# Kernel optimization log

Hardware: AMD Instinct MI355X
Metric: run time of the kernel (lower is better)

The kernel has to match this reference:

```python
import jax, jax.numpy as jnp
import numpy as np

B, N, C, H, D, M = 8, 4096, 512, 8, 64, 16
TOPK = 3
TAU = 0.1
DIV_REG = 0.01


def setup_inputs() -> dict:
    key = jax.random.key(0)
    ks = jax.random.split(key, 12)
    w = lambda i, shape: 0.02 * jax.random.normal(ks[i], shape, dtype=jnp.float32)
    return {
        "x": jax.random.normal(ks[0], (B, N, C), dtype=jnp.float32),
        "W_qkv": w(1, (C, 3 * C)),                    # qkv_bias=False
        "W_proj": w(2, (C, C)), "b_proj": jnp.zeros((C,), jnp.float32),
        "W_rspec": w(3, (C, H * M)), "b_rspec": jnp.zeros((H * M,), jnp.float32),
        "W_rspat": w(4, (C, H * M)), "b_rspat": jnp.zeros((H * M,), jnp.float32),
        "K_spec": w(5, (H, M, D)),                    # prototype banks (EMA buffers)
        "K_spat": w(6, (H, M, D)),
        "W_tok": w(7, (D, D)), "b_tok": jnp.zeros((D,), jnp.float32),
        "W_prot": w(8, (D, D)), "b_prot": jnp.zeros((D,), jnp.float32),
    }


def topk_mask_from_logits(logits, k):
    # keep top-k of softmax probs along last axis, renormalize
    vals = jax.lax.top_k(logits, k)[0]
    thresh = vals[..., -1:]
    mask = (logits >= thresh).astype(logits.dtype)
    probs = jax.nn.softmax(logits, axis=-1) * mask
    denom = jnp.maximum(jnp.sum(probs, axis=-1, keepdims=True), 1e-6)
    return probs / denom


def _l2norm(a, eps):
    return a / jnp.maximum(jnp.linalg.norm(a, axis=-1, keepdims=True), eps)


def reference(x, W_qkv, W_proj, b_proj, W_rspec, b_rspec, W_rspat, b_rspat,
              K_spec, K_spat, W_tok, b_tok, W_prot, b_prot):
    # qkv: [B,N,3C] -> q,k,v each [B,H,N,D]
    qkv = (x @ W_qkv).reshape(B, N, 3, H, D).transpose(2, 0, 3, 1, 4)
    q, _k, v = qkv[0], qkv[1], qkv[2]

    # routing logits [B,H,N,M] -> top-k masked probs
    r_spec = topk_mask_from_logits(
        (x @ W_rspec + b_rspec).reshape(B, N, H, M).transpose(0, 2, 1, 3), TOPK)
    r_spat = topk_mask_from_logits(
        (x @ W_rspat + b_rspat).reshape(B, N, H, M).transpose(0, 2, 1, 3), TOPK)

    # effective keys from prototype banks: [B,H,N,D]
    K_eff = (jnp.einsum('bhnm,hmd->bhnd', r_spec, K_spec)
             + jnp.einsum('bhnm,hmd->bhnd', r_spat, K_spat))
    K_norm = jax.nn.softmax(K_eff, axis=-2)          # softmax over tokens N

    # linear attention reorder: context [B,H,D,D], then Q @ context
    context = jnp.einsum('bhnd,bhne->bhde', K_norm, v)
    out = jnp.einsum('bhnd,bhde->bhne', q, context)  # note: scale unused in source
    out = out.transpose(0, 2, 1, 3).reshape(B, N, C) @ W_proj + b_proj

    # ---- contrastive aux loss ----
    t_n = _l2norm(v @ W_tok + b_tok, 1e-12)          # [B,H,N,D]
    p_spec_n = _l2norm(K_spec @ W_prot + b_prot, 1e-12)
    p_spat_n = _l2norm(K_spat @ W_prot + b_prot, 1e-12)
    sim_spec = jnp.einsum('bhnd,hmd->bhnm', t_n, p_spec_n)
    sim_spat = jnp.einsum('bhnd,hmd->bhnm', t_n, p_spat_n)
    pos_spec = jnp.sum(sim_spec * r_spec, axis=-1)
    pos_spat = jnp.sum(sim_spat * r_spat, axis=-1)
    loss_spec = -jnp.mean(pos_spec / TAU - jax.nn.logsumexp(sim_spec / TAU, axis=-1))
    loss_spat = -jnp.mean(pos_spat / TAU - jax.nn.logsumexp(sim_spat / TAU, axis=-1))
    contrastive_loss = 0.5 * (loss_spec + loss_spat)

    def diversity_loss(P):
        h, m, _d = P.shape
        p = P / jnp.maximum(jnp.linalg.norm(P, axis=-1, keepdims=True), 1e-6)
        sim = jnp.einsum('hmd,hnd->hmn', p, p)
        mask = 1.0 - jnp.eye(m, dtype=P.dtype)[None]
        return jnp.sum(sim * mask) / (h * m * (m - 1) + 1e-6)

    diversity = DIV_REG * (diversity_loss(K_spec) + diversity_loss(K_spat))
    return out, contrastive_loss, diversity
```

## Files before the change

kernel.cpp:

```cpp
#include <hip/hip_runtime.h>
#include <math.h>

#define B_ 8
#define N_ 4096
#define C_ 512
#define H_ 8
#define D_ 64
#define M_ 16
#define BN_TOK (B_*N_)
#define TAU_ 0.1f

typedef short s8v __attribute__((ext_vector_type(8)));
typedef float f4v __attribute__((ext_vector_type(4)));
typedef unsigned short u16;

__device__ __forceinline__ float wave_reduce_sum(float v){
  #pragma unroll
  for (int o = 32; o > 0; o >>= 1) v += __shfl_xor(v, o);
  return v;
}

__device__ __forceinline__ unsigned short f2b(float f){
  unsigned int u = __float_as_uint(f);
  u += 0x7fffu + ((u >> 16) & 1u);
  return (unsigned short)(u >> 16);
}

__device__ __forceinline__ float b2f(u16 b){
  return __uint_as_float(((unsigned int)b) << 16);
}

__device__ __forceinline__ s8v pack8(const float* f){
  s8v r;
  #pragma unroll
  for (int e = 0; e < 8; ++e) r[e] = (short)f2b(f[e]);
  return r;
}

__device__ __forceinline__ void gload16(const u16* g, u16* l){
  __builtin_amdgcn_global_load_lds(
      (const __attribute__((address_space(1))) unsigned int*)g,
      (__attribute__((address_space(3))) unsigned int*)l, 16, 0, 0);
}

__global__ __launch_bounds__(256) void prep_all(const float* __restrict__ x, u16* __restrict__ xb,
                                                const float* __restrict__ W_qkv,
                                                const float* __restrict__ W_rspec,
                                                const float* __restrict__ W_rspat,
                                                const float* __restrict__ W_proj,
                                                u16* __restrict__ Wqk,
                                                u16* __restrict__ Wt_v,
                                                u16* __restrict__ Wt_r,
                                                u16* __restrict__ Wt_p){
  const int bid = blockIdx.x;
  const int t = threadIdx.x;
  if (bid < 1024) {
    const int n8 = (BN_TOK*C_)/8;
    for (int i = bid * 256 + t; i < n8; i += 1024*256) {
      const float4* p = (const float4*)(x + (size_t)i * 8);
      float4 a = p[0], b = p[1];
      float f[8] = {a.x,a.y,a.z,a.w,b.x,b.y,b.z,b.w};
      *(s8v*)(xb + (size_t)i * 8) = pack8(f);
    }
    return;
  }
  if (bid < 1536) {
    const int k = bid - 1024;
    Wqk[(size_t)k*512 + t]       = f2b(W_qkv[(size_t)k*1536 + t]);
    Wqk[(size_t)k*512 + t + 256] = f2b(W_qkv[(size_t)k*1536 + t + 256]);
    return;
  }
  const int r = bid - 1536;
  const float* src; int ld, coff, n; u16* dst;
  if (r < 512)       { src = W_qkv;   ld = 1536; coff = 1024; n = r;        dst = Wt_v; }
  else if (r < 640)  { src = W_rspec; ld = 128;  coff = 0;    n = r - 512;  dst = Wt_r; }
  else if (r < 768)  { src = W_rspat; ld = 128;  coff = 0;    n = r - 640;  dst = Wt_r + 128*512; }
  else               { src = W_proj;  ld = 512;  coff = 0;    n = r - 768;  dst = Wt_p; }
  dst[(size_t)n*512 + t]       = f2b(src[(size_t)t*ld + coff + n]);
  dst[(size_t)n*512 + t + 256] = f2b(src[(size_t)(t+256)*ld + coff + n]);
}

template<int MODE>
__global__ __launch_bounds__(256) void gemm_bt(const u16* __restrict__ A,
                                               const u16* __restrict__ Bt,
                                               const float* __restrict__ bias,
                                               void* __restrict__ C,
                                               u16* __restrict__ C2,
                                               int K, int lda, int ldc, int ldc2,
                                               int split, int bt_bstride) {
  __shared__ __align__(16) u16 Asm[2][2][128*32];
  __shared__ __align__(16) u16 Bsm[2][2][128*32];
  const int tid = threadIdx.x;
  const int lane = tid & 63, w = tid >> 6;
  const int bm = blockIdx.x * 128, bn = blockIdx.y * 128;

  const int lrow = lane >> 2;
  const int kch  = ((lane & 3) ^ ((lane >> 3) & 3)) << 3;

  const u16* Btb = Bt + (size_t)(bm >> 12) * bt_bstride;
  const u16* Ag0 = A   + (size_t)(bm + w*16 + lrow) * lda + kch;
  const u16* Ag1 = Ag0 + (size_t)64 * lda;
  const u16* Bg0 = Btb + (size_t)(bn + w*16 + lrow) * K + kch;
  const u16* Bg1 = Bg0 + (size_t)64 * K;
  const int l0 = (w*16)*32, l1 = (w*16+64)*32;

  const int lm = lane & 15, lg = lane >> 4;
  const int w0 = (w >> 1) * 64, c0 = (w & 1) * 64;
  const int xs = (lg ^ ((lm >> 1) & 3)) << 3;

  const int NSTEP = K >> 6;

  f4v acc[4][4];
  #pragma unroll
  for (int i = 0; i < 4; ++i)
    #pragma unroll
    for (int j = 0; j < 4; ++j) acc[i][j] = (f4v){0.f,0.f,0.f,0.f};

  #define STAGE(buf, tt)                                        \
    gload16(Ag0 + (tt)*64,      &Asm[buf][0][l0]);              \
    gload16(Ag1 + (tt)*64,      &Asm[buf][0][l1]);              \
    gload16(Ag0 + (tt)*64 + 32, &Asm[buf][1][l0]);              \
    gload16(Ag1 + (tt)*64 + 32, &Asm[buf][1][l1]);              \
    gload16(Bg0 + (tt)*64,      &Bsm[buf][0][l0]);              \
    gload16(Bg1 + (tt)*64,      &Bsm[buf][0][l1]);              \
    gload16(Bg0 + (tt)*64 + 32, &Bsm[buf][1][l0]);              \
    gload16(Bg1 + (tt)*64 + 32, &Bsm[buf][1][l1]);

  STAGE(0, 0)
  STAGE(1, 1)

  int cur = 0;
  for (int k = 0; k < NSTEP; ++k) {
    if (k < NSTEP - 1) asm volatile("s_waitcnt vmcnt(8)" ::: "memory");
    else               asm volatile("s_waitcnt vmcnt(0)" ::: "memory");
    __builtin_amdgcn_s_barrier();
    __builtin_amdgcn_sched_barrier(0);

    #pragma unroll
    for (int h = 0; h < 2; ++h) {
      s8v af[4], bf_[4];
      #pragma unroll
      for (int i = 0; i < 4; ++i) af[i]  = *(const s8v*)&Asm[cur][h][(w0 + 16*i + lm)*32 + xs];
      #pragma unroll
      for (int j = 0; j < 4; ++j) bf_[j] = *(const s8v*)&Bsm[cur][h][(c0 + 16*j + lm)*32 + xs];
      #pragma unroll
      for (int i = 0; i < 4; ++i)
        #pragma unroll
        for (int j = 0; j < 4; ++j)
          acc[i][j] = __builtin_amdgcn_mfma_f32_16x16x32_bf16(af[i], bf_[j], acc[i][j], 0, 0, 0);
    }

    __builtin_amdgcn_sched_barrier(0);
    __builtin_amdgcn_s_barrier();
    if (k + 2 < NSTEP) {
      STAGE(cur, k + 2)
    }
    __builtin_amdgcn_sched_barrier(0);
    cur ^= 1;
  }
  #undef STAGE

  #pragma unroll
  for (int j = 0; j < 4; ++j) {
    const int col = bn + c0 + 16*j + lm;
    const float bj = (MODE == 0 && bias) ? bias[col] : 0.f;
    #pragma unroll
    for (int i = 0; i < 4; ++i) {
      const int row = bm + w0 + 16*i + 4*lg;
      #pragma unroll
      for (int r = 0; r < 4; ++r) {
        if (MODE == 2 && bn >= split)
          C2[(size_t)(row + r) * ldc2 + (col - split)] = f2b(acc[i][j][r]);
        else if (MODE == 1 || MODE == 2)
          ((u16*)C)[(size_t)(row + r) * ldc + col] = f2b(acc[i][j][r]);
        else
          ((float*)C)[(size_t)(row + r) * ldc + col] = acc[i][j][r] + bj;
      }
    }
  }
}

__global__ __launch_bounds__(256) void router_topk(const u16* __restrict__ logits,
                            const float* __restrict__ b_rspec, const float* __restrict__ b_rspat,
                            u16* __restrict__ rb_spec, u16* __restrict__ rb_spat) {
  int t = blockIdx.x * blockDim.x + threadIdx.x;
  if (t >= BN_TOK * H_ * 2) return;
  int route = t & 1, h = (t >> 1) & 7, bn = t >> 4;
  int b = bn >> 12, n = bn & 4095;
  const u16* lg = logits + (size_t)bn*256 + route*128 + h*16;
  const float* bias = (route ? b_rspat : b_rspec) + h*16;
  float v[16];
  #pragma unroll
  for (int m=0;m<16;++m) v[m] = b2f(lg[m]) + bias[m];
  float m1=-1e30f, m2=-1e30f, m3=-1e30f;
  #pragma unroll
  for (int m=0;m<16;++m){
    float x=v[m];
    if (x>m1){m3=m2;m2=m1;m1=x;}
    else if (x>m2){m3=m2;m2=x;}
    else if (x>m3){m3=x;}
  }
  float S=0.f, Sm=0.f, e[16];
  #pragma unroll
  for (int m=0;m<16;++m){ e[m]=expf(v[m]-m1); S+=e[m]; if (v[m]>=m3) Sm+=e[m]; }
  float denom = fmaxf(Sm/S, 1e-6f);
  float inv = 1.f/(S*denom);
  size_t idx = (((size_t)b*H_ + h)*N_ + n)*16;
  u16* rb  = (route ? rb_spat : rb_spec) + idx;
  #pragma unroll
  for (int m=0;m<16;++m) {
    float val = (v[m] >= m3) ? e[m]*inv : 0.f;
    rb[m] = f2b(val);
  }
}

__global__ __launch_bounds__(256) void context_mfma(const u16* __restrict__ rb_spec, const u16* __restrict__ rb_spat,
                               const float* __restrict__ K_spec, const float* __restrict__ K_spat,
                               const u16* __restrict__ vb, u16* __restrict__ pctx, float* __restrict__ pZ) {
  const int chunk = blockIdx.x & 15, bh = blockIdx.x >> 4;
  const int b = bh >> 3, h = bh & 7;
  const int tid = threadIdx.x;
  const int lane = tid & 63, w = tid >> 6;
  const int lm = lane & 15, lg = lane >> 4;

  __shared__ __align__(16) unsigned short Kc[64*32];
  __shared__ __align__(16) unsigned short Rs[64*32];
  __shared__ __align__(16) unsigned short Vt[64*64];
  __shared__ __align__(16) unsigned short Ps[64*64];
  __shared__ float Zs[256];

  {
    int d = tid & 63, c = tid >> 6;
    float f[8];
    #pragma unroll
    for (int u = 0; u < 8; ++u) {
      int k = c*8 + u;
      f[u] = (k < 16) ? K_spec[h*1024 + k*64 + d] : K_spat[h*1024 + (k-16)*64 + d];
    }
    *(s8v*)&Kc[d*32 + ((c ^ (d&3)) << 3)] = pack8(f);
  }

  const u16* rsg = rb_spec + ((size_t)bh*N_ + chunk*256)*16;
  const u16* rtg = rb_spat + ((size_t)bh*N_ + chunk*256)*16;
  const u16* vbase = vb + h*64;
  const size_t tokbase = (size_t)b*N_ + chunk*256;

  f4v acc2[4];
  #pragma unroll
  for (int j = 0; j < 4; ++j) acc2[j] = (f4v){0.f,0.f,0.f,0.f};
  float zreg[4] = {0.f,0.f,0.f,0.f};

  for (int t0 = 0; t0 < 4; ++t0) {
    __syncthreads();
    {
      int n = tid & 63, c = tid >> 6;
      const u16* src = (c < 2 ? rsg : rtg) + ((size_t)(t0*64 + n))*16 + (c&1)*8;
      *(s8v*)&Rs[n*32 + ((c ^ (n&3)) << 3)] = *(const s8v*)src;
    }
    {
      int n = tid & 63, eq = tid >> 6;
      const u16* src = vbase + (tokbase + t0*64 + n)*512 + eq*16;
      u16 f[16];
      *(s8v*)&f[0] = ((const s8v*)src)[0];
      *(s8v*)&f[8] = ((const s8v*)src)[1];
      #pragma unroll
      for (int u = 0; u < 16; ++u) {
        int e = eq*16 + u;
        Vt[e*64 + ((((n>>3) ^ (e&7)) << 3) | (n&7))] = f[u];
      }
    }
    __syncthreads();
    {
      s8v a1 = *(const s8v*)&Rs[(16*w + lm)*32 + ((lg ^ (lm&3)) << 3)];
      #pragma unroll
      for (int j = 0; j < 4; ++j) {
        s8v b1 = *(const s8v*)&Kc[(16*j + lm)*32 + ((lg ^ (lm&3)) << 3)];
        f4v c1 = (f4v){0.f,0.f,0.f,0.f};
        c1 = __builtin_amdgcn_mfma_f32_16x16x32_bf16(a1, b1, c1, 0, 0, 0);
        float p0 = expf(c1[0]), p1 = expf(c1[1]), p2 = expf(c1[2]), p3 = expf(c1[3]);
        float zz = p0 + p1 + p2 + p3;
        zz += __shfl_xor(zz, 16); zz += __shfl_xor(zz, 32);
        zreg[j] += zz;
        int d = 16*j + lm;
        int n0w = 16*w + 4*lg;
        Ps[d*64 + (((((n0w  )>>3) ^ (d&7)) << 3) | ((n0w  )&7))] = f2b(p0);
        Ps[d*64 + (((((n0w+1)>>3) ^ (d&7)) << 3) | ((n0w+1)&7))] = f2b(p1);
        Ps[d*64 + (((((n0w+2)>>3) ^ (d&7)) << 3) | ((n0w+2)&7))] = f2b(p2);
        Ps[d*64 + (((((n0w+3)>>3) ^ (d&7)) << 3) | ((n0w+3)&7))] = f2b(p3);
      }
    }
    __syncthreads();
    #pragma unroll
    for (int kb = 0; kb < 2; ++kb) {
      s8v a2 = *(const s8v*)&Vt[(16*w + lm)*64 + (((kb*4 + lg) ^ (lm&7)) << 3)];
      #pragma unroll
      for (int j = 0; j < 4; ++j) {
        s8v b2 = *(const s8v*)&Ps[(16*j + lm)*64 + (((kb*4 + lg) ^ (lm&7)) << 3)];
        acc2[j] = __builtin_amdgcn_mfma_f32_16x16x32_bf16(a2, b2, acc2[j], 0, 0, 0);
      }
    }
  }
  u16* pc = pctx + (size_t)(bh*16 + chunk)*4096;
  #pragma unroll
  for (int j = 0; j < 4; ++j) {
    #pragma unroll
    for (int r = 0; r < 4; ++r)
      pc[(16*w + 4*lg + r)*64 + 16*j + lm] = f2b(acc2[j][r]);
    if (lg == 0) Zs[w*64 + 16*j + lm] = zreg[j];
  }
  __syncthreads();
  if (tid < 64)
    pZ[(size_t)(bh*16 + chunk)*64 + tid] = Zs[tid] + Zs[64+tid] + Zs[128+tid] + Zs[192+tid];
}

__global__ __launch_bounds__(256) void context_reduce(const u16* __restrict__ pctx, const float* __restrict__ pZ,
                              float* __restrict__ ctx) {
  const int gid = blockIdx.x * 256 + threadIdx.x;
  const int bh = gid >> 12, e = (gid >> 6) & 63, d = gid & 63;
  float z = 0.f, s = 0.f;
  for (int c = 0; c < 16; ++c) {
    z += pZ[(size_t)(bh*16 + c)*64 + d];
    s += b2f(pctx[(size_t)(bh*16 + c)*4096 + e*64 + d]);
  }
  ctx[(size_t)bh*4096 + e*64 + d] = s / z;
}

__global__ __launch_bounds__(256) void cwt_kernel(const float* __restrict__ ctx, const u16* __restrict__ Wt_p,
                                                  u16* __restrict__ CWt) {
  const int bh = blockIdx.x >> 3, oct = blockIdx.x & 7;
  const int b = bh >> 3, h = bh & 7;
  const int tid = threadIdx.x;
  __shared__ float ctxS[64*64];
  __shared__ u16 WsL[64*64];
  {
    int e = tid >> 2, dq = tid & 3;
    const float4* src = (const float4*)(ctx + (size_t)bh*4096 + e*64 + dq*16);
    float4* dst = (float4*)(ctxS + e*64 + dq*16);
    dst[0] = src[0]; dst[1] = src[1]; dst[2] = src[2]; dst[3] = src[3];
  }
  const int c0 = oct * 64;
  {
    int cl = tid >> 2, eq = tid & 3;
    const s8v* src = (const s8v*)(Wt_p + (size_t)(c0 + cl)*512 + h*64 + eq*16);
    *(s8v*)&WsL[cl*64 + eq*16]     = src[0];
    *(s8v*)&WsL[cl*64 + eq*16 + 8] = src[1];
  }
  __syncthreads();
  const int d = tid & 63, cq = tid >> 6;
  for (int ci = 0; ci < 16; ++ci) {
    int cl = cq*16 + ci;
    float acc = 0.f;
    #pragma unroll
    for (int e = 0; e < 64; ++e)
      acc = fmaf(ctxS[e*64 + d], b2f(WsL[cl*64 + e]), acc);
    CWt[((size_t)b*512 + (c0 + cl))*512 + h*64 + d] = f2b(acc);
  }
}

__global__ __launch_bounds__(64) void protnorm_div(const float* __restrict__ K_spec, const float* __restrict__ K_spat,
                               const float* __restrict__ W_prot, const float* __restrict__ b_prot,
                               float* __restrict__ pnorm, float* __restrict__ pdiv) {
  const int bid = blockIdx.x;
  const int e = threadIdx.x;
  if (bid < 256) {
    int route = bid >> 7, hm = bid & 127;
    const float* Km = (route ? K_spat : K_spec) + hm*64;
    __shared__ float kv[64];
    kv[e] = Km[e];
    __syncthreads();
    float acc = b_prot[e];
    for (int dcol = 0; dcol < 64; ++dcol) acc = fmaf(kv[dcol], W_prot[dcol*64 + e], acc);
    float n2 = wave_reduce_sum(acc*acc);
    pnorm[(size_t)bid*64 + e] = acc / fmaxf(sqrtf(n2), 1e-12f);
    return;
  }
  const int db = bid - 256;
  int route = db >> 3, h = db & 7;
  const float* Km = (route ? K_spat : K_spec) + h*16*64;
  float s = 0.f, selfsum = 0.f;
  for (int m = 0; m < 16; ++m) {
    float x = Km[m*64 + e];
    float n2 = wave_reduce_sum(x*x);
    float p = x / fmaxf(sqrtf(n2), 1e-6f);
    s += p; selfsum += p*p;
  }
  float off = wave_reduce_sum(s*s - selfsum);
  if (e == 0) pdiv[db] = off;
}

__global__ __launch_bounds__(256) void contrastive_mfma(const u16* __restrict__ vb,
                                   const u16* __restrict__ rb_spec, const u16* __restrict__ rb_spat,
                                   const float* __restrict__ W_tok, const float* __restrict__ b_tok,
                                   const float* __restrict__ pnorm, float* __restrict__ pcontr) {
  const int tile = blockIdx.x & 255;
  const int h = blockIdx.x >> 8;
  const int t0 = tile * 128;
  const int b = t0 >> 12;
  const int n0 = t0 & 4095;
  const int tid = threadIdx.x;
  const int lane = tid & 63, w = tid >> 6;
  const int lm = lane & 15, lg = lane >> 4;

  __shared__ __align__(16) unsigned short Usm[128*72];
  __shared__ __align__(16) unsigned short Wsm[64*72];
  __shared__ __align__(16) unsigned short Psm[32*72];
  __shared__ float nrmS[128];
  __shared__ float btkS[64];
  __shared__ float bred[2][4];
  float* Uf = (float*)Usm;

  {
    const int vr = tid >> 1, vh = tid & 1;
    const u16* vg = vb + (size_t)(b*N_ + n0 + vr)*512 + h*64 + vh*32;
    #pragma unroll
    for (int c = 0; c < 4; ++c) *(s8v*)&Usm[vr*72 + vh*32 + c*8] = ((const s8v*)vg)[c];
  }
  {
    const int e = tid & 63, kh = tid >> 6;
    float f[16];
    #pragma unroll
    for (int rr = 0; rr < 16; ++rr) f[rr] = W_tok[(size_t)(kh*16+rr)*64 + e];
    *(s8v*)&Wsm[e*72 + kh*16]     = pack8(&f[0]);
    *(s8v*)&Wsm[e*72 + kh*16 + 8] = pack8(&f[8]);
  }
  if (tid < 128) {
    const int proto = tid >> 2, q4 = tid & 3;
    const int src = (proto < 16) ? (h*16 + proto) : (128 + h*16 + (proto-16));
    const float* pg = pnorm + (size_t)src*64 + q4*16;
    float f[16];
    #pragma unroll
    for (int i = 0; i < 4; ++i) {
      float4 v4 = ((const float4*)pg)[i];
      f[4*i]=v4.x; f[4*i+1]=v4.y; f[4*i+2]=v4.z; f[4*i+3]=v4.w;
    }
    *(s8v*)&Psm[proto*72 + q4*16]     = pack8(&f[0]);
    *(s8v*)&Psm[proto*72 + q4*16 + 8] = pack8(&f[8]);
  }
  if (tid < 64) btkS[tid] = b_tok[tid];
  __syncthreads();

  f4v acc[2][4];
  #pragma unroll
  for (int i=0;i<2;++i)
    #pragma unroll
    for (int j=0;j<4;++j) acc[i][j] = (f4v){0.f,0.f,0.f,0.f};
  {
    s8v bf0[4], bf1[4];
    #pragma unroll
    for (int j=0;j<4;++j) {
      bf0[j] = *(const s8v*)&Wsm[(j*16+lm)*72 + lg*8];
      bf1[j] = *(const s8v*)&Wsm[(j*16+lm)*72 + 32 + lg*8];
    }
    #pragma unroll
    for (int i=0;i<2;++i) {
      s8v af0 = *(const s8v*)&Usm[(w*32+16*i+lm)*72 + lg*8];
      s8v af1 = *(const s8v*)&Usm[(w*32+16*i+lm)*72 + 32 + lg*8];
      #pragma unroll
      for (int j=0;j<4;++j) {
        acc[i][j] = __builtin_amdgcn_mfma_f32_16x16x32_bf16(af0, bf0[j], acc[i][j], 0, 0, 0);
        acc[i][j] = __builtin_amdgcn_mfma_f32_16x16x32_bf16(af1, bf1[j], acc[i][j], 0, 0, 0);
      }
    }
  }
  #pragma unroll
  for (int i=0;i<2;++i) {
    #pragma unroll
    for (int r=0;r<4;++r) {
      float s = 0.f;
      #pragma unroll
      for (int j=0;j<4;++j) {
        float val = acc[i][j][r] + btkS[j*16+lm];
        acc[i][j][r] = val;
        s += val*val;
      }
      s += __shfl_xor(s,1); s += __shfl_xor(s,2); s += __shfl_xor(s,4); s += __shfl_xor(s,8);
      if (lm == 0) nrmS[w*32 + 16*i + lg*4 + r] = s;
    }
  }
  #pragma unroll
  for (int i=0;i<2;++i)
    #pragma unroll
    for (int j=0;j<4;++j)
      #pragma unroll
      for (int r=0;r<4;++r)
        Usm[(w*32+16*i+lg*4+r)*72 + j*16+lm] = f2b(acc[i][j][r]);
  __syncthreads();

  f4v acc2[2][2];
  #pragma unroll
  for (int i=0;i<2;++i)
    #pragma unroll
    for (int j=0;j<2;++j) acc2[i][j] = (f4v){0.f,0.f,0.f,0.f};
  {
    s8v bf0[2], bf1[2];
    #pragma unroll
    for (int j=0;j<2;++j) {
      bf0[j] = *(const s8v*)&Psm[(j*16+lm)*72 + lg*8];
      bf1[j] = *(const s8v*)&Psm[(j*16+lm)*72 + 32 + lg*8];
    }
    #pragma unroll
    for (int i=0;i<2;++i) {
      s8v af0 = *(const s8v*)&Usm[(w*32+16*i+lm)*72 + lg*8];
      s8v af1 = *(const s8v*)&Usm[(w*32+16*i+lm)*72 + 32 + lg*8];
      #pragma unroll
      for (int j=0;j<2;++j) {
        acc2[i][j] = __builtin_amdgcn_mfma_f32_16x16x32_bf16(af0, bf0[j], acc2[i][j], 0, 0, 0);
        acc2[i][j] = __builtin_amdgcn_mfma_f32_16x16x32_bf16(af1, bf1[j], acc2[i][j], 0, 0, 0);
      }
    }
  }
  #pragma unroll
  for (int i=0;i<2;++i)
    #pragma unroll
    for (int j=0;j<2;++j)
      #pragma unroll
      for (int r=0;r<4;++r)
        Uf[(w*32+16*i+lg*4+r)*36 + j*16+lm] = acc2[i][j][r];
  __syncthreads();

  float l = 0.f;
  {
    const int tt = tid >> 1, route = tid & 1;
    float inv = 1.f / fmaxf(sqrtf(nrmS[tt]), 1e-12f);
    const u16* rg = (route ? rb_spat : rb_spec) + (((size_t)b*H_ + h)*N_ + n0 + tt)*16;
    float s0[16];
    #pragma unroll
    for (int m=0;m<16;++m) s0[m] = Uf[tt*36 + route*16 + m]*inv;
    float pos = 0.f, mx = -1e30f;
    #pragma unroll
    for (int m=0;m<16;++m) {
      pos += s0[m]*b2f(rg[m]);
      mx = fmaxf(mx, s0[m]);
    }
    float z = 0.f;
    #pragma unroll
    for (int m=0;m<16;++m) z += expf((s0[m]-mx)/TAU_);
    l = pos/TAU_ - (mx/TAU_ + logf(z));
  }
  float lspec = (tid & 1) ? 0.f : l;
  float lspat = (tid & 1) ? l : 0.f;
  lspec = wave_reduce_sum(lspec);
  lspat = wave_reduce_sum(lspat);
  if (lane == 0) { bred[0][w]=lspec; bred[1][w]=lspat; }
  __syncthreads();
  if (tid == 0) {
    pcontr[2*blockIdx.x]     = bred[0][0]+bred[0][1]+bred[0][2]+bred[0][3];
    pcontr[2*blockIdx.x + 1] = bred[1][0]+bred[1][1]+bred[1][2]+bred[1][3];
  }
}

__global__ __launch_bounds__(256) void finalize_kernel(const float* __restrict__ pcontr,
                                                       const float* __restrict__ pdiv,
                                                       float* __restrict__ tail) {
  __shared__ float red[2][4];
  const int tid = threadIdx.x, lane = tid & 63, w = tid >> 6;
  float ls = 0.f, lt = 0.f;
  for (int k = tid; k < 2048; k += 256) { ls += pcontr[2*k]; lt += pcontr[2*k + 1]; }
  ls = wave_reduce_sum(ls);
  lt = wave_reduce_sum(lt);
  if (lane == 0) { red[0][w] = ls; red[1][w] = lt; }
  __syncthreads();
  if (tid == 0) {
    float sspec = red[0][0]+red[0][1]+red[0][2]+red[0][3];
    float sspat = red[1][0]+red[1][1]+red[1][2]+red[1][3];
    float dspec = 0.f, dspat = 0.f;
    for (int k = 0; k < 8; ++k) { dspec += pdiv[k]; dspat += pdiv[8+k]; }
    float loss_spec = -(sspec / (float)(B_*H_*N_));
    float loss_spat = -(sspat / (float)(B_*H_*N_));
    float denom = (float)(H_*M_*(M_-1)) + 1e-6f;
    tail[0] = 0.5f*(loss_spec + loss_spat);
    tail[1] = 0.01f * (dspec/denom + dspat/denom);
  }
}

extern "C" void kernel_launch(void* const* d_in, const int* in_sizes, int n_in,
                              void* d_out, int out_size, void* d_ws, size_t ws_size,
                              hipStream_t stream) {
  const float* x       = (const float*)d_in[0];
  const float* W_qkv   = (const float*)d_in[1];
  const float* W_proj  = (const float*)d_in[2];
  const float* b_proj  = (const float*)d_in[3];
  const float* W_rspec = (const float*)d_in[4];
  const float* b_rspec = (const float*)d_in[5];
  const float* W_rspat = (const float*)d_in[6];
  const float* b_rspat = (const float*)d_in[7];
  const float* K_spec  = (const float*)d_in[8];
  const float* K_spat  = (const float*)d_in[9];
  const float* W_tok   = (const float*)d_in[10];
  const float* b_tok   = (const float*)d_in[11];
  const float* W_prot  = (const float*)d_in[12];
  const float* b_prot  = (const float*)d_in[13];
  float* out = (float*)d_out;

  float* ws = (float*)d_ws;
  u16*   vb      = (u16*)ws;
  u16*   logits  = (u16*)(ws + 8388608);
  u16*   pctx    = (u16*)(ws + 8388608);
  float* pZ      = ws + 8388608 + 4194304;
  u16*   rb_spec = (u16*)(ws + 12648448);
  u16*   rb_spat = (u16*)(ws + 14745600);
  u16*   xb      = (u16*)(ws + 16842752);
  u16*   Wqk     = (u16*)(ws + 25231360);
  u16*   Wt_v    = (u16*)(ws + 25362432);
  u16*   Wt_r    = (u16*)(ws + 25493504);
  u16*   Wt_p    = (u16*)(ws + 25559040);
  float* ctxb    = ws + 25690112;
  float* pnorm   = ws + 25952256;
  float* pcontr  = ws + 25968640;
  float* pdiv    = ws + 25972736;
  u16*   CWt     = (u16*)(ws + 25972752);
  u16*   W2t     = (u16*)(ws + 27021328);

  dim3 blk256(256);

  prep_all<<<2816, blk256, 0, stream>>>(x, xb, W_qkv, W_rspec, W_rspat, W_proj, Wqk, Wt_v, Wt_r, Wt_p);

  gemm_bt<2><<<dim3(256,6), blk256, 0, stream>>>(xb, Wt_v, nullptr, vb, logits,
                                                 512, 512, 512, 256, 512, 0);
  router_topk<<<2048, blk256, 0, stream>>>(logits, b_rspec, b_rspat, rb_spec, rb_spat);
  context_mfma<<<1024, blk256, 0, stream>>>(rb_spec, rb_spat, K_spec, K_spat, vb, pctx, pZ);
  context_reduce<<<1024, blk256, 0, stream>>>(pctx, pZ, ctxb);
  cwt_kernel<<<512, blk256, 0, stream>>>(ctxb, Wt_p, CWt);
  gemm_bt<1><<<dim3(32,4), blk256, 0, stream>>>(CWt, Wqk, nullptr, W2t, nullptr,
                                                512, 512, 512, 0, 1 << 30, 0);
  protnorm_div<<<272, dim3(64), 0, stream>>>(K_spec, K_spat, W_prot, b_prot, pnorm, pdiv);
  contrastive_mfma<<<2048, blk256, 0, stream>>>(vb, rb_spec, rb_spat, W_tok, b_tok, pnorm, pcontr);
  gemm_bt<0><<<dim3(256,4), blk256, 0, stream>>>(xb, W2t, b_proj, out, nullptr,
                                                 512, 512, 512, 0, 1 << 30, 512*512);
  finalize_kernel<<<1, blk256, 0, stream>>>(pcontr, pdiv, out + 16777216);
}
```

Before: 306.0 us.

## Fuse router top-k into consumers and fold context reduction into cwt kernel

Removes the standalone router_topk kernel. The top-k softmax routing weights are now recomputed from the bf16 logits inside both context_mfma and contrastive_mfma. The context_reduce kernel is also dropped: cwt_kernel sums the 16 partial contexts and normalizers itself and applies 1/Z at the output. This cuts two launches and the round trip of the routing and context buffers through global memory, at the cost of computing top-k twice and doing a strided gather of the partials in cwt_kernel. The workspace is re-laid out so pctx no longer aliases logits, which are now still read later.

Result: slower. 314.7 us (+2.9%).

```diff
diff --git a/kernel.cpp b/kernel.cpp
--- a/kernel.cpp
+++ b/kernel.cpp
@@ -35,6 +35,24 @@
   #pragma unroll
   for (int e = 0; e < 8; ++e) r[e] = (short)f2b(f[e]);
   return r;
+}
+
+__device__ __forceinline__ void topk16(const float* v, float* out){
+  float m1=-1e30f, m2=-1e30f, m3=-1e30f;
+  #pragma unroll
+  for (int m=0;m<16;++m){
+    float x=v[m];
+    if (x>m1){m3=m2;m2=m1;m1=x;}
+    else if (x>m2){m3=m2;m2=x;}
+    else if (x>m3){m3=x;}
+  }
+  float S=0.f, Sm=0.f, e[16];
+  #pragma unroll
+  for (int m=0;m<16;++m){ e[m]=expf(v[m]-m1); S+=e[m]; if (v[m]>=m3) Sm+=e[m]; }
+  float denom = fmaxf(Sm/S, 1e-6f);
+  float inv = 1.f/(S*denom);
+  #pragma unroll
+  for (int m=0;m<16;++m) out[m] = (v[m] >= m3) ? e[m]*inv : 0.f;
 }
 
 __device__ __forceinline__ void gload16(const u16* g, u16* l){
@@ -180,41 +198,8 @@
   }
 }
 
-__global__ __launch_bounds__(256) void router_topk(const u16* __restrict__ logits,
-                            const float* __restrict__ b_rspec, const float* __restrict__ b_rspat,
-                            u16* __restrict__ rb_spec, u16* __restrict__ rb_spat) {
-  int t = blockIdx.x * blockDim.x + threadIdx.x;
-  if (t >= BN_TOK * H_ * 2) return;
-  int route = t & 1, h = (t >> 1) & 7, bn = t >> 4;
-  int b = bn >> 12, n = bn & 4095;
-  const u16* lg = logits + (size_t)bn*256 + route*128 + h*16;
-  const float* bias = (route ? b_rspat : b_rspec) + h*16;
-  float v[16];
-  #pragma unroll
-  for (int m=0;m<16;++m) v[m] = b2f(lg[m]) + bias[m];
-  float m1=-1e30f, m2=-1e30f, m3=-1e30f;
-  #pragma unroll
-  for (int m=0;m<16;++m){
-    float x=v[m];
-    if (x>m1){m3=m2;m2=m1;m1=x;}
-    else if (x>m2){m3=m2;m2=x;}
-    else if (x>m3){m3=x;}
-  }
-  float S=0.f, Sm=0.f, e[16];
-  #pragma unroll
-  for (int m=0;m<16;++m){ e[m]=expf(v[m]-m1); S+=e[m]; if (v[m]>=m3) Sm+=e[m]; }
-  float denom = fmaxf(Sm/S, 1e-6f);
-  float inv = 1.f/(S*denom);
-  size_t idx = (((size_t)b*H_ + h)*N_ + n)*16;
-  u16* rb  = (route ? rb_spat : rb_spec) + idx;
-  #pragma unroll
-  for (int m=0;m<16;++m) {
-    float val = (v[m] >= m3) ? e[m]*inv : 0.f;
-    rb[m] = f2b(val);
-  }
-}
-
-__global__ __launch_bounds__(256) void context_mfma(const u16* __restrict__ rb_spec, const u16* __restrict__ rb_spat,
+__global__ __launch_bounds__(256) void context_mfma(const u16* __restrict__ logits,
+                               const float* __restrict__ b_rspec, const float* __restrict__ b_rspat,
                                const float* __restrict__ K_spec, const float* __restrict__ K_spat,
                                const u16* __restrict__ vb, u16* __restrict__ pctx, float* __restrict__ pZ) {
   const int chunk = blockIdx.x & 15, bh = blockIdx.x >> 4;
@@ -224,7 +209,7 @@
   const int lm = lane & 15, lg = lane >> 4;
 
   __shared__ __align__(16) unsigned short Kc[64*32];
-  __shared__ __align__(16) unsigned short Rs[64*32];
+  __shared__ __align__(16) unsigned short Rall[256*32];
   __shared__ __align__(16) unsigned short Vt[64*64];
   __shared__ __align__(16) unsigned short Ps[64*64];
   __shared__ float Zs[256];
@@ -239,9 +224,22 @@
     }
     *(s8v*)&Kc[d*32 + ((c ^ (d&3)) << 3)] = pack8(f);
   }
-
-  const u16* rsg = rb_spec + ((size_t)bh*N_ + chunk*256)*16;
-  const u16* rtg = rb_spat + ((size_t)bh*N_ + chunk*256)*16;
+  {
+    const int n = tid;
+    const size_t tok = (size_t)b*N_ + chunk*256 + n;
+    #pragma unroll
+    for (int route = 0; route < 2; ++route) {
+      const u16* lgp = logits + tok*256 + route*128 + h*16;
+      const float* bias = (route ? b_rspat : b_rspec) + h*16;
+      float v[16], rr[16];
+      #pragma unroll
+      for (int m=0;m<16;++m) v[m] = b2f(lgp[m]) + bias[m];
+      topk16(v, rr);
+      *(s8v*)&Rall[n*32 + (((route*2  ) ^ (n&3)) << 3)] = pack8(&rr[0]);
+      *(s8v*)&Rall[n*32 + (((route*2+1) ^ (n&3)) << 3)] = pack8(&rr[8]);
+    }
+  }
+
   const u16* vbase = vb + h*64;
   const size_t tokbase = (size_t)b*N_ + chunk*256;
 
@@ -252,11 +250,6 @@
 
   for (int t0 = 0; t0 < 4; ++t0) {
     __syncthreads();
-    {
-      int n = tid & 63, c = tid >> 6;
-      const u16* src = (c < 2 ? rsg : rtg) + ((size_t)(t0*64 + n))*16 + (c&1)*8;
-      *(s8v*)&Rs[n*32 + ((c ^ (n&3)) << 3)] = *(const s8v*)src;
-    }
     {
       int n = tid & 63, eq = tid >> 6;
       const u16* src = vbase + (tokbase + t0*64 + n)*512 + eq*16;
@@ -271,7 +264,7 @@
     }
     __syncthreads();
     {
-      s8v a1 = *(const s8v*)&Rs[(16*w + lm)*32 + ((lg ^ (lm&3)) << 3)];
+      s8v a1 = *(const s8v*)&Rall[(t0*64 + 16*w + lm)*32 + ((lg ^ (lm&3)) << 3)];
       #pragma unroll
       for (int j = 0; j < 4; ++j) {
         s8v b1 = *(const s8v*)&Kc[(16*j + lm)*32 + ((lg ^ (lm&3)) << 3)];
@@ -313,30 +306,29 @@
     pZ[(size_t)(bh*16 + chunk)*64 + tid] = Zs[tid] + Zs[64+tid] + Zs[128+tid] + Zs[192+tid];
 }
 
-__global__ __launch_bounds__(256) void context_reduce(const u16* __restrict__ pctx, const float* __restrict__ pZ,
-                              float* __restrict__ ctx) {
-  const int gid = blockIdx.x * 256 + threadIdx.x;
-  const int bh = gid >> 12, e = (gid >> 6) & 63, d = gid & 63;
-  float z = 0.f, s = 0.f;
-  for (int c = 0; c < 16; ++c) {
-    z += pZ[(size_t)(bh*16 + c)*64 + d];
-    s += b2f(pctx[(size_t)(bh*16 + c)*4096 + e*64 + d]);
-  }
-  ctx[(size_t)bh*4096 + e*64 + d] = s / z;
-}
-
-__global__ __launch_bounds__(256) void cwt_kernel(const float* __restrict__ ctx, const u16* __restrict__ Wt_p,
-                                                  u16* __restrict__ CWt) {
+__global__ __launch_bounds__(256) void cwt_kernel(const u16* __restrict__ pctx, const float* __restrict__ pZ,
+                                                  const u16* __restrict__ Wt_p, u16* __restrict__ CWt) {
   const int bh = blockIdx.x >> 3, oct = blockIdx.x & 7;
   const int b = bh >> 3, h = bh & 7;
   const int tid = threadIdx.x;
   __shared__ float ctxS[64*64];
+  __shared__ float Zsum[64];
   __shared__ u16 WsL[64*64];
+  if (tid < 64) {
+    float z = 0.f;
+    for (int c = 0; c < 16; ++c) z += pZ[(size_t)(bh*16 + c)*64 + tid];
+    Zsum[tid] = z;
+  }
   {
     int e = tid >> 2, dq = tid & 3;
-    const float4* src = (const float4*)(ctx + (size_t)bh*4096 + e*64 + dq*16);
-    float4* dst = (float4*)(ctxS + e*64 + dq*16);
-    dst[0] = src[0]; dst[1] = src[1]; dst[2] = src[2]; dst[3] = src[3];
+    #pragma unroll
+    for (int dd = 0; dd < 16; ++dd) {
+      int d = dq*16 + dd;
+      float s = 0.f;
+      for (int c = 0; c < 16; ++c)
+        s += b2f(pctx[(size_t)(bh*16 + c)*4096 + e*64 + d]);
+      ctxS[e*64 + d] = s;
+    }
   }
   const int c0 = oct * 64;
   {
@@ -347,13 +339,14 @@
   }
   __syncthreads();
   const int d = tid & 63, cq = tid >> 6;
+  const float invZ = 1.f / Zsum[d];
   for (int ci = 0; ci < 16; ++ci) {
     int cl = cq*16 + ci;
     float acc = 0.f;
     #pragma unroll
     for (int e = 0; e < 64; ++e)
       acc = fmaf(ctxS[e*64 + d], b2f(WsL[cl*64 + e]), acc);
-    CWt[((size_t)b*512 + (c0 + cl))*512 + h*64 + d] = f2b(acc);
+    CWt[((size_t)b*512 + (c0 + cl))*512 + h*64 + d] = f2b(acc * invZ);
   }
 }
 
@@ -389,7 +382,8 @@
 }
 
 __global__ __launch_bounds__(256) void contrastive_mfma(const u16* __restrict__ vb,
-                                   const u16* __restrict__ rb_spec, const u16* __restrict__ rb_spat,
+                                   const u16* __restrict__ logits,
+                                   const float* __restrict__ b_rspec, const float* __restrict__ b_rspat,
                                    const float* __restrict__ W_tok, const float* __restrict__ b_tok,
                                    const float* __restrict__ pnorm, float* __restrict__ pcontr) {
   const int tile = blockIdx.x & 255;
@@ -522,14 +516,20 @@
   {
     const int tt = tid >> 1, route = tid & 1;
     float inv = 1.f / fmaxf(sqrtf(nrmS[tt]), 1e-12f);
-    const u16* rg = (route ? rb_spat : rb_spec) + (((size_t)b*H_ + h)*N_ + n0 + tt)*16;
+    const size_t tok = (size_t)b*N_ + n0 + tt;
+    const u16* lgp = logits + tok*256 + route*128 + h*16;
+    const float* bias = (route ? b_rspat : b_rspec) + h*16;
+    float vv[16], rv[16];
+    #pragma unroll
+    for (int m=0;m<16;++m) vv[m] = b2f(lgp[m]) + bias[m];
+    topk16(vv, rv);
     float s0[16];
     #pragma unroll
     for (int m=0;m<16;++m) s0[m] = Uf[tt*36 + route*16 + m]*inv;
     float pos = 0.f, mx = -1e30f;
     #pragma unroll
     for (int m=0;m<16;++m) {
-      pos += s0[m]*b2f(rg[m]);
+      pos += s0[m]*rv[m];
       mx = fmaxf(mx, s0[m]);
     }
     float z = 0.f;
@@ -595,21 +595,18 @@
   float* ws = (float*)d_ws;
   u16*   vb      = (u16*)ws;
   u16*   logits  = (u16*)(ws + 8388608);
-  u16*   pctx    = (u16*)(ws + 8388608);
-  float* pZ      = ws + 8388608 + 4194304;
-  u16*   rb_spec = (u16*)(ws + 12648448);
-  u16*   rb_spat = (u16*)(ws + 14745600);
-  u16*   xb      = (u16*)(ws + 16842752);
-  u16*   Wqk     = (u16*)(ws + 25231360);
-  u16*   Wt_v    = (u16*)(ws + 25362432);
-  u16*   Wt_r    = (u16*)(ws + 25493504);
-  u16*   Wt_p    = (u16*)(ws + 25559040);
-  float* ctxb    = ws + 25690112;
-  float* pnorm   = ws + 25952256;
-  float* pcontr  = ws + 25968640;
-  float* pdiv    = ws + 25972736;
-  u16*   CWt     = (u16*)(ws + 25972752);
-  u16*   W2t     = (u16*)(ws + 27021328);
+  u16*   pctx    = (u16*)(ws + 12582912);
+  float* pZ      = ws + 14680064;
+  u16*   xb      = (u16*)(ws + 14745600);
+  u16*   Wqk     = (u16*)(ws + 23134208);
+  u16*   Wt_v    = (u16*)(ws + 23265280);
+  u16*   Wt_r    = (u16*)(ws + 23396352);
+  u16*   Wt_p    = (u16*)(ws + 23461888);
+  float* pnorm   = ws + 23592960;
+  float* pcontr  = ws + 23609344;
+  float* pdiv    = ws + 23613440;
+  u16*   CWt     = (u16*)(ws + 23613456);
+  u16*   W2t     = (u16*)(ws + 24662032);
 
   dim3 blk256(256);
 
@@ -617,14 +614,12 @@
 
   gemm_bt<2><<<dim3(256,6), blk256, 0, stream>>>(xb, Wt_v, nullptr, vb, logits,
                                                  512, 512, 512, 256, 512, 0);
-  router_topk<<<2048, blk256, 0, stream>>>(logits, b_rspec, b_rspat, rb_spec, rb_spat);
-  context_mfma<<<1024, blk256, 0, stream>>>(rb_spec, rb_spat, K_spec, K_spat, vb, pctx, pZ);
-  context_reduce<<<1024, blk256, 0, stream>>>(pctx, pZ, ctxb);
-  cwt_kernel<<<512, blk256, 0, stream>>>(ctxb, Wt_p, CWt);
+  context_mfma<<<1024, blk256, 0, stream>>>(logits, b_rspec, b_rspat, K_spec, K_spat, vb, pctx, pZ);
+  cwt_kernel<<<512, blk256, 0, stream>>>(pctx, pZ, Wt_p, CWt);
   gemm_bt<1><<<dim3(32,4), blk256, 0, stream>>>(CWt, Wqk, nullptr, W2t, nullptr,
                                                 512, 512, 512, 0, 1 << 30, 0);
   protnorm_div<<<272, dim3(64), 0, stream>>>(K_spec, K_spat, W_prot, b_prot, pnorm, pdiv);
-  contrastive_mfma<<<2048, blk256, 0, stream>>>(vb, rb_spec, rb_spat, W_tok, b_tok, pnorm, pcontr);
+  contrastive_mfma<<<2048, blk256, 0, stream>>>(vb, logits, b_rspec, b_rspat, W_tok, b_tok, pnorm, pcontr);
   gemm_bt<0><<<dim3(256,4), blk256, 0, stream>>>(xb, W2t, b_proj, out, nullptr,
                                                  512, 512, 512, 0, 1 << 30, 512*512);
   finalize_kernel<<<1, blk256, 0, stream>>>(pcontr, pdiv, out + 16777216);
```
